# Optimization experiments

Hardware: AMD Instinct MI355X
Metric: run time of the kernel (lower is better)

## Reference

```python
import jax, jax.numpy as jnp
import numpy as np

N = 50000      # n_nodes
E = 800000     # n_edges
IN_NF = 64     # in_node_nf
HID = 128      # hidden_nf
OUT_NF = 64    # out_node_nf
L = 4          # n_layers
EH = HID // 2  # edge MLP hidden width (edge_nf_ratio=2)
C = 1.0        # aggregation scaling constant


def _w(k, shape):
    # fan-in scaled init (matches nn.Linear scale roughly)
    return jax.random.normal(k, shape, dtype=jnp.float32) / np.sqrt(shape[-2]).astype(np.float32)


def setup_inputs() -> dict:
    key = jax.random.key(0)
    ks = jax.random.split(key, 10)
    h = jax.random.normal(ks[0], (N, IN_NF), dtype=jnp.float32)
    edges = jax.random.randint(ks[1], (2, E), 0, N, dtype=jnp.int32)
    return {
        "h": h,
        "edges": edges,
        "W_in": _w(ks[2], (IN_NF, HID)),
        "b_in": jnp.zeros((HID,), jnp.float32),
        # stacked per-layer GCL params, leading dim L
        "eW1": _w(ks[3], (L, 2 * HID, EH)),
        "eb1": jnp.zeros((L, EH), jnp.float32),
        "eW2": _w(ks[4], (L, EH, EH)),
        "eb2": jnp.zeros((L, EH), jnp.float32),
        "nW1": _w(ks[5], (L, HID + EH, HID)),
        "nb1": jnp.zeros((L, HID), jnp.float32),
        "nW2": _w(ks[6], (L, HID, HID)),
        "nb2": jnp.zeros((L, HID), jnp.float32),
        "W_out": _w(ks[7], (HID, OUT_NF)),
        "b_out": jnp.zeros((OUT_NF,), jnp.float32),
    }


def reference(h, edges, W_in, b_in, eW1, eb1, eW2, eb2, nW1, nb1, nW2, nb2, W_out, b_out):
    row, col = edges[0], edges[1]
    h = h @ W_in + b_in  # [N, HID] embedding_in

    def layer(hc, p):
        w1, b1, w2, b2, m1, c1, m2, c2 = p
        # edge model: gather endpoints, concat, 2-layer SiLU MLP
        m = jnp.concatenate([hc[row], hc[col]], axis=1)          # [E, 2*HID]
        m = jax.nn.silu(m @ w1 + b1)                             # [E, EH]
        m = jax.nn.silu(m @ w2 + b2)                             # [E, EH]
        # node model: scatter-sum messages to source nodes, scale by C
        agg = jax.ops.segment_sum(m, row, num_segments=N) * C    # [N, EH]
        z = jnp.concatenate([hc, agg], axis=1)                   # [N, HID+EH]
        z = jax.nn.silu(z @ m1 + c1)
        z = z @ m2 + c2                                          # [N, HID]
        return hc + z, None  # residual=True

    h, _ = jax.lax.scan(layer, h, (eW1, eb1, eW2, eb2, nW1, nb1, nW2, nb2))
    return h @ W_out + b_out  # [N, OUT_NF] embedding_out
```

## Files before the change

kernel.cpp:

```cpp
#include <hip/hip_runtime.h>
#include <hip/hip_bf16.h>
#include <cstdint>
#include <cstddef>

#define N_NODES 50000
#define N_EDGES 800000
#define NR      50048
#define NBKT    196
#define BSH     8
#define BCHUNK  2048
#define CAP     6144

typedef __attribute__((ext_vector_type(8))) short short8;
typedef __attribute__((ext_vector_type(4))) float floatx4;
typedef __attribute__((ext_vector_type(4))) unsigned int uintx4;

__device__ inline float bf2f(unsigned short u) {
    union { unsigned int i; float f; } v; v.i = ((unsigned int)u) << 16; return v.f;
}
__device__ inline unsigned short f2bf(float f) {
    union { float f; unsigned int i; } v; v.f = f;
    unsigned int u = v.i;
    return (unsigned short)((u + 0x7FFFu + ((u >> 16) & 1u)) >> 16);
}
__device__ inline unsigned int f2bf_pk(float a, float b) {
    __hip_bfloat162 h2 = __float22bfloat162_rn(make_float2(a, b));
    return *reinterpret_cast<unsigned int*>(&h2);
}
__device__ inline float2 bf2f2(unsigned int u) {
    union { unsigned int i; float f; } lo, hi;
    lo.i = u << 16;
    hi.i = u & 0xFFFF0000u;
    return make_float2(lo.f, hi.f);
}
__device__ inline float silu_f(float x) {
    float e = __expf(-x);
    return x * __builtin_amdgcn_rcpf(1.0f + e);
}

__device__ inline int block_excl_scan_256(int v, int* buf) {
    int tid = threadIdx.x;
    buf[tid] = v;
    __syncthreads();
    #pragma unroll
    for (int off = 1; off < 256; off <<= 1) {
        int t = (tid >= off) ? buf[tid - off] : 0;
        __syncthreads();
        buf[tid] += t;
        __syncthreads();
    }
    return buf[tid] - v;
}

__device__ inline void pack_std(const float* __restrict__ src,
                                unsigned short* __restrict__ dst,
                                int NOUT, long j) {
    int i = (int)(j & 7);
    long rest = j >> 3;
    int n = (int)(rest % NOUT);
    int kb = (int)(rest / NOUT);
    dst[j] = f2bf(src[(long)(kb * 8 + i) * NOUT + n]);
}

#define NH0   (N_NODES * 64L)
#define SW_IN 8192L
#define SW_OUT 8192L
#define SW1   16384L
#define SE2   4096L
#define SN1   24576L
#define SN2   16384L
#define SB    128L
#define PERL  (SW1 + SE2 + SN1 + SN2 + SB)
#define PACK_TOTAL (NH0 + SW_IN + SW_OUT + 4 * PERL)

__global__ __launch_bounds__(256) void pack_kernel(
    const float* __restrict__ h0, const float* __restrict__ W_in,
    const float* __restrict__ W_out, const float* __restrict__ eW1,
    const float* __restrict__ eb1, const float* __restrict__ eW2,
    const float* __restrict__ nW1, const float* __restrict__ nW2,
    unsigned short* __restrict__ h0bf, unsigned short* __restrict__ Winp,
    unsigned short* __restrict__ Woutp, unsigned short* __restrict__ W1p,
    unsigned short* __restrict__ eW2p, unsigned short* __restrict__ nW1p,
    unsigned short* __restrict__ nW2p, float* __restrict__ biasP)
{
    long idx = (long)blockIdx.x * 256 + threadIdx.x;
    if (idx >= PACK_TOTAL) return;
    long j = idx;
    if (j < NH0) { h0bf[j] = f2bf(h0[j]); return; }
    j -= NH0;
    if (j < SW_IN) { pack_std(W_in, Winp, 128, j); return; }
    j -= SW_IN;
    if (j < SW_OUT) { pack_std(W_out, Woutp, 64, j); return; }
    j -= SW_OUT;
    int l = (int)(j / PERL);
    long r = j % PERL;
    if (r < SW1) {
        int i = (int)(r & 7);
        int n = (int)((r >> 3) & 127);
        int kb = (int)(r >> 10);
        int k = kb * 8 + i;
        const float* w = eW1 + (long)l * 256 * 64;
        float v = (n < 64) ? w[(long)k * 64 + n] : w[(long)(128 + k) * 64 + (n - 64)];
        W1p[(long)l * SW1 + r] = f2bf(v);
        return;
    }
    r -= SW1;
    if (r < SE2) { pack_std(eW2 + (long)l * 4096, eW2p + (long)l * SE2, 64, r); return; }
    r -= SE2;
    if (r < SN1) { pack_std(nW1 + (long)l * 24576, nW1p + (long)l * SN1, 128, r); return; }
    r -= SN1;
    if (r < SN2) { pack_std(nW2 + (long)l * 16384, nW2p + (long)l * SN2, 128, r); return; }
    r -= SN2;
    biasP[(long)l * 128 + r] = (r < 64) ? eb1[(long)l * 64 + r] : 0.0f;
}

__global__ __launch_bounds__(256) void hist_k(const int* __restrict__ erow,
                                              int* __restrict__ countB, int E) {
    __shared__ int c[NBKT];
    for (int i = threadIdx.x; i < NBKT; i += 256) c[i] = 0;
    __syncthreads();
    int j = blockIdx.x * BCHUNK + threadIdx.x;
    #pragma unroll
    for (int i = 0; i < BCHUNK / 256; i++, j += 256)
        if (j < E) atomicAdd(&c[erow[j] >> BSH], 1);
    __syncthreads();
    for (int i = threadIdx.x; i < NBKT; i += 256)
        if (c[i]) atomicAdd(&countB[i], c[i]);
}

__global__ __launch_bounds__(256) void bucket_scan_k(const int* __restrict__ countB,
                                                     int* __restrict__ bucketBase,
                                                     int* __restrict__ bucketCursor) {
    __shared__ int buf[256];
    int tid = threadIdx.x;
    int v = (tid < NBKT) ? countB[tid] : 0;
    int excl = block_excl_scan_256(v, buf);
    if (tid < NBKT) {
        bucketBase[tid] = excl;
        bucketCursor[tid] = excl;
    }
    if (tid == NBKT - 1) bucketBase[NBKT] = excl + v;
}

__global__ __launch_bounds__(256) void bin_k(
    const int* __restrict__ erow, const int* __restrict__ ecol,
    int* __restrict__ bucketCursor, int2* __restrict__ binned, int E)
{
    __shared__ int2 staged[BCHUNK];
    __shared__ int cnt[NBKT];
    __shared__ int binStart[NBKT];
    __shared__ int gbase[NBKT];
    __shared__ int scanbuf[256];
    const int tid = threadIdx.x;
    const int base = blockIdx.x * BCHUNK;
    const int nloc = min(BCHUNK, E - base);

    for (int i = tid; i < NBKT; i += 256) cnt[i] = 0;
    __syncthreads();

    int2 ed[BCHUNK / 256];
    int  bo[BCHUNK / 256];
    #pragma unroll
    for (int i = 0; i < BCHUNK / 256; i++) {
        int jl = i * 256 + tid;
        if (jl < nloc) {
            int j = base + jl;
            int r = erow[j], c = ecol[j];
            ed[i] = make_int2(r, c);
            int b = r >> BSH;
            int off = atomicAdd(&cnt[b], 1);
            bo[i] = (b << 12) | off;
        } else bo[i] = -1;
    }
    __syncthreads();

    int v = (tid < NBKT) ? cnt[tid] : 0;
    int excl = block_excl_scan_256(v, scanbuf);
    if (tid < NBKT) binStart[tid] = excl;
    if (tid < NBKT && v > 0) gbase[tid] = atomicAdd(&bucketCursor[tid], v);
    __syncthreads();

    #pragma unroll
    for (int i = 0; i < BCHUNK / 256; i++) {
        if (bo[i] >= 0)
            staged[binStart[bo[i] >> 12] + (bo[i] & 0xFFF)] = ed[i];
    }
    __syncthreads();

    for (int j = tid; j < nloc; j += 256) {
        int2 e = staged[j];
        int b = e.x >> BSH;
        binned[gbase[b] + (j - binStart[b])] = e;
    }
}

__global__ __launch_bounds__(256) void sort_k(
    const int2* __restrict__ binned, const int* __restrict__ bucketBase,
    int2* __restrict__ eidx)
{
    __shared__ int2 st[CAP];
    __shared__ int cnt[256];
    __shared__ int cur[256];
    __shared__ int scanbuf[256];
    const int b = blockIdx.x;
    const int tid = threadIdx.x;
    const int s0 = bucketBase[b];
    int n = bucketBase[b + 1] - s0;
    if (n > CAP) n = CAP;

    cnt[tid] = 0;
    __syncthreads();
    for (int j = tid; j < n; j += 256) {
        int2 e = binned[s0 + j];
        st[j] = e;
        atomicAdd(&cnt[e.x & 255], 1);
    }
    __syncthreads();
    int excl = block_excl_scan_256(cnt[tid], scanbuf);
    cur[tid] = excl;
    __syncthreads();
    for (int j = tid; j < n; j += 256) {
        int2 e = st[j];
        int pos = atomicAdd(&cur[e.x & 255], 1);
        eidx[s0 + pos] = e;
    }
}

__global__ __launch_bounds__(256) void edge_fused_k(
    const int2* __restrict__ eidx,
    const unsigned short* __restrict__ P,
    const unsigned short* __restrict__ Bp,
    const float* __restrict__ b2, float* __restrict__ agg, int E)
{
    __shared__ float M2s[64 * 68];
    __shared__ int ridS[64];
    __shared__ short segStartS[66];
    __shared__ int nsegS;
    const int tid = threadIdx.x;
    const int wave = tid >> 6;
    const int lane = tid & 63;
    const int lrow = lane & 15;
    const int quad = lane >> 4;
    const int e0 = blockIdx.x * 64;
    const int el = wave * 16 + lrow;
    const int e = e0 + el;

    short8 af0 = {0, 0, 0, 0, 0, 0, 0, 0};
    short8 af1 = af0;
    if (e < E) {
        int2 rc = eidx[e];
        int rr = rc.x, cc = rc.y;
        if (quad == 0) ridS[el] = rr;
        const uintx4* pt = (const uintx4*)(P + (size_t)rr * 128 + quad * 8);
        const uintx4* pb = (const uintx4*)(P + (size_t)cc * 128 + 64 + quad * 8);
        uintx4 t0 = pt[0], t1 = pt[4];
        uintx4 b0 = pb[0], b1 = pb[4];
        const unsigned int* t0u = (const unsigned int*)&t0;
        const unsigned int* t1u = (const unsigned int*)&t1;
        const unsigned int* b0u = (const unsigned int*)&b0;
        const unsigned int* b1u = (const unsigned int*)&b1;
        unsigned int o0[4], o1[4];
        #pragma unroll
        for (int i = 0; i < 4; i++) {
            float2 a0 = bf2f2(t0u[i]), c0 = bf2f2(b0u[i]);
            o0[i] = f2bf_pk(silu_f(a0.x + c0.x), silu_f(a0.y + c0.y));
            float2 a1 = bf2f2(t1u[i]), c1 = bf2f2(b1u[i]);
            o1[i] = f2bf_pk(silu_f(a1.x + c1.x), silu_f(a1.y + c1.y));
        }
        af0 = *(const short8*)o0;
        af1 = *(const short8*)o1;
    } else if (quad == 0) {
        ridS[el] = -1;
    }

    floatx4 acc[4];
    #pragma unroll
    for (int i = 0; i < 4; i++) acc[i] = (floatx4){0, 0, 0, 0};
    #pragma unroll
    for (int nt = 0; nt < 4; nt++) {
        short8 bf0 = *(const short8*)(Bp + (size_t)((0 * 4 + quad) * 64 + nt * 16 + lrow) * 8);
        acc[nt] = __builtin_amdgcn_mfma_f32_16x16x32_bf16(af0, bf0, acc[nt], 0, 0, 0);
        short8 bf1 = *(const short8*)(Bp + (size_t)((1 * 4 + quad) * 64 + nt * 16 + lrow) * 8);
        acc[nt] = __builtin_amdgcn_mfma_f32_16x16x32_bf16(af1, bf1, acc[nt], 0, 0, 0);
    }

    #pragma unroll
    for (int nt = 0; nt < 4; nt++) {
        int n = nt * 16 + lrow;
        float bv = b2[n];
        #pragma unroll
        for (int r = 0; r < 4; r++) {
            int el2 = wave * 16 + quad * 4 + r;
            M2s[el2 * 68 + n] = silu_f(acc[nt][r] + bv);
        }
    }
    __syncthreads();

    if (tid < 64) {
        bool st = (ridS[tid] >= 0) && (tid == 0 || ridS[tid] != ridS[tid - 1]);
        unsigned long long m = __ballot(st);
        if (st) {
            int pos = __popcll(m & ((1ull << tid) - 1));
            segStartS[pos] = (short)tid;
        }
        if (tid == 0) {
            int ns = __popcll(m);
            nsegS = ns;
            int nvalid = E - e0;
            if (nvalid > 64) nvalid = 64;
            segStartS[ns] = (short)nvalid;
        }
    }
    __syncthreads();

    {
        int f = tid & 63;
        int g = tid >> 6;
        int ns = nsegS;
        for (int j = g; j < ns; j += 4) {
            int a = segStartS[j], b = segStartS[j + 1];
            float s = 0.0f;
            for (int el2 = a; el2 < b; el2++) s += M2s[el2 * 68 + f];
            int rv = ridS[a];
            if (j == 0 || j == ns - 1)
                atomicAdd(&agg[(size_t)rv * 64 + f], s);
            else
                agg[(size_t)rv * 64 + f] = s;
        }
    }
}

#define SROW 264
template<int FINAL>
__global__ __launch_bounds__(512) void node_fused_k(
    const unsigned short* __restrict__ hbf, const float* __restrict__ agg,
    const unsigned short* __restrict__ W1, const float* __restrict__ b1,
    const unsigned short* __restrict__ W2, const float* __restrict__ b2,
    const unsigned short* __restrict__ B3, const float* __restrict__ bias3,
    float* __restrict__ hFT, unsigned short* __restrict__ hB,
    unsigned short* __restrict__ Pout, float* __restrict__ outF,
    float* __restrict__ aggZ, int M)
{
    __shared__ unsigned short S[64 * SROW];
    const int tid = threadIdx.x;
    const int m0 = blockIdx.x * 64;
    const int wave = tid >> 6;
    const int lane = tid & 63;
    const int lrow = lane & 15;
    const int quad = lane >> 4;
    const int g = wave >> 1;
    const int h = wave & 1;
    const int row0 = m0 + g * 16 + quad * 4;
    const int elb = g * 16 + quad * 4;

    short8 afa0, afa1;
    {
        const float* ap = agg + (size_t)(m0 + g * 16 + lrow) * 64;
        floatx4 q0 = *(const floatx4*)(ap + quad * 8);
        floatx4 q1 = *(const floatx4*)(ap + quad * 8 + 4);
        floatx4 q2 = *(const floatx4*)(ap + 32 + quad * 8);
        floatx4 q3 = *(const floatx4*)(ap + 32 + quad * 8 + 4);
        unsigned int c0[4] = { f2bf_pk(q0[0], q0[1]), f2bf_pk(q0[2], q0[3]),
                               f2bf_pk(q1[0], q1[1]), f2bf_pk(q1[2], q1[3]) };
        unsigned int c1[4] = { f2bf_pk(q2[0], q2[1]), f2bf_pk(q2[2], q2[3]),
                               f2bf_pk(q3[0], q3[1]), f2bf_pk(q3[2], q3[3]) };
        afa0 = *(const short8*)c0;
        afa1 = *(const short8*)c1;
    }

    floatx4 res4[4];
    #pragma unroll
    for (int j = 0; j < 4; j++) {
        int n = (4 * h + j) * 16 + lrow;
        res4[j] = *(const floatx4*)(hFT + (size_t)n * NR + row0);
    }

    for (int t = tid; t < 64 * 16; t += 512) {
        int rr = t >> 4, c = t & 15;
        int row = m0 + rr;
        uintx4 val = {0, 0, 0, 0};
        if (row < M) val = *(const uintx4*)(hbf + (size_t)row * 128 + c * 8);
        *(uintx4*)(&S[rr * SROW + c * 8]) = val;
    }
    __syncthreads();

    if (!FINAL) {
        floatx4 z = {0, 0, 0, 0};
        for (int t = tid; t < 64 * 16; t += 512) {
            int rr = t >> 4, c = t & 15;
            int row = m0 + rr;
            if (row < M) *(floatx4*)(aggZ + (size_t)row * 64 + c * 4) = z;
        }
    }

    const unsigned short* arow = &S[(g * 16 + lrow) * SROW];

    floatx4 acc[4];
    #pragma unroll
    for (int i = 0; i < 4; i++) acc[i] = (floatx4){0, 0, 0, 0};
    #pragma unroll
    for (int kt = 0; kt < 4; kt++) {
        short8 afrag = *(const short8*)(arow + kt * 32 + quad * 8);
        int kb = kt * 4 + quad;
        #pragma unroll
        for (int j = 0; j < 4; j++) {
            int n = (4 * h + j) * 16 + lrow;
            short8 bfrag = *(const short8*)(W1 + (size_t)(kb * 128 + n) * 8);
            acc[j] = __builtin_amdgcn_mfma_f32_16x16x32_bf16(afrag, bfrag, acc[j], 0, 0, 0);
        }
    }
    #pragma unroll
    for (int j = 0; j < 4; j++) {
        int n = (4 * h + j) * 16 + lrow;
        short8 b4 = *(const short8*)(W1 + (size_t)((16 + quad) * 128 + n) * 8);
        acc[j] = __builtin_amdgcn_mfma_f32_16x16x32_bf16(afa0, b4, acc[j], 0, 0, 0);
        short8 b5 = *(const short8*)(W1 + (size_t)((20 + quad) * 128 + n) * 8);
        acc[j] = __builtin_amdgcn_mfma_f32_16x16x32_bf16(afa1, b5, acc[j], 0, 0, 0);
    }

    #pragma unroll
    for (int j = 0; j < 4; j++) {
        int n = (4 * h + j) * 16 + lrow;
        float bv = b1[n];
        unsigned int p01 = f2bf_pk(silu_f(acc[j][0] + bv), silu_f(acc[j][1] + bv));
        unsigned int p23 = f2bf_pk(silu_f(acc[j][2] + bv), silu_f(acc[j][3] + bv));
        S[(elb + 0) * SROW + 128 + n] = (unsigned short)(p01 & 0xFFFF);
        S[(elb + 1) * SROW + 128 + n] = (unsigned short)(p01 >> 16);
        S[(elb + 2) * SROW + 128 + n] = (unsigned short)(p23 & 0xFFFF);
        S[(elb + 3) * SROW + 128 + n] = (unsigned short)(p23 >> 16);
    }
    __syncthreads();

    floatx4 acc2[4];
    #pragma unroll
    for (int i = 0; i < 4; i++) acc2[i] = (floatx4){0, 0, 0, 0};
    #pragma unroll
    for (int kt = 0; kt < 4; kt++) {
        short8 afrag = *(const short8*)(arow + 128 + kt * 32 + quad * 8);
        int kb = kt * 4 + quad;
        #pragma unroll
        for (int j = 0; j < 4; j++) {
            int n = (4 * h + j) * 16 + lrow;
            short8 bfrag = *(const short8*)(W2 + (size_t)(kb * 128 + n) * 8);
            acc2[j] = __builtin_amdgcn_mfma_f32_16x16x32_bf16(afrag, bfrag, acc2[j], 0, 0, 0);
        }
    }

    #pragma unroll
    for (int j = 0; j < 4; j++) {
        int n = (4 * h + j) * 16 + lrow;
        float bv = b2[n];
        floatx4 v4;
        #pragma unroll
        for (int r = 0; r < 4; r++) v4[r] = acc2[j][r] + bv + res4[j][r];
        unsigned int p01 = f2bf_pk(v4[0], v4[1]);
        unsigned int p23 = f2bf_pk(v4[2], v4[3]);
        S[(elb + 0) * SROW + n] = (unsigned short)(p01 & 0xFFFF);
        S[(elb + 1) * SROW + n] = (unsigned short)(p01 >> 16);
        S[(elb + 2) * SROW + n] = (unsigned short)(p23 & 0xFFFF);
        S[(elb + 3) * SROW + n] = (unsigned short)(p23 >> 16);
        if (!FINAL && row0 < M)
            *(floatx4*)(hFT + (size_t)n * NR + row0) = v4;
    }
    __syncthreads();

    constexpr int NT3 = FINAL ? 2 : 4;
    constexpr int NO3 = FINAL ? 64 : 128;
    floatx4 acc3[NT3];
    #pragma unroll
    for (int i = 0; i < NT3; i++) acc3[i] = (floatx4){0, 0, 0, 0};
    #pragma unroll
    for (int kt = 0; kt < 4; kt++) {
        short8 afrag = *(const short8*)(arow + kt * 32 + quad * 8);
        int kb = kt * 4 + quad;
        #pragma unroll
        for (int j = 0; j < NT3; j++) {
            int n = (NT3 * h + j) * 16 + lrow;
            short8 bfrag = *(const short8*)(B3 + (size_t)(kb * NO3 + n) * 8);
            acc3[j] = __builtin_amdgcn_mfma_f32_16x16x32_bf16(afrag, bfrag, acc3[j], 0, 0, 0);
        }
    }
    #pragma unroll
    for (int j = 0; j < NT3; j++) {
        int n = (NT3 * h + j) * 16 + lrow;
        float bv = bias3[n];
        if (FINAL) {
            #pragma unroll
            for (int r = 0; r < 4; r++)
                ((float*)(&S[(elb + r) * SROW + 128]))[n] = acc3[j][r] + bv;
        } else {
            unsigned int p01 = f2bf_pk(acc3[j][0] + bv, acc3[j][1] + bv);
            unsigned int p23 = f2bf_pk(acc3[j][2] + bv, acc3[j][3] + bv);
            S[(elb + 0) * SROW + 128 + n] = (unsigned short)(p01 & 0xFFFF);
            S[(elb + 1) * SROW + 128 + n] = (unsigned short)(p01 >> 16);
            S[(elb + 2) * SROW + 128 + n] = (unsigned short)(p23 & 0xFFFF);
            S[(elb + 3) * SROW + 128 + n] = (unsigned short)(p23 >> 16);
        }
    }
    __syncthreads();

    if (FINAL) {
        for (int t = tid; t < 64 * 16; t += 512) {
            int rr = t >> 4, c = t & 15;
            int row = m0 + rr;
            if (row < M)
                *(floatx4*)(outF + (size_t)row * 64 + c * 4) =
                    *(const floatx4*)((const float*)(&S[rr * SROW + 128]) + c * 4);
        }
    } else {
        for (int t = tid; t < 64 * 32; t += 512) {
            int rr = t >> 5, c = t & 31;
            int row = m0 + rr;
            if (row < M) {
                if (c < 16)
                    *(uintx4*)(hB + (size_t)row * 128 + c * 8) =
                        *(const uintx4*)(&S[rr * SROW + c * 8]);
                else
                    *(uintx4*)(Pout + (size_t)row * 128 + (c - 16) * 8) =
                        *(const uintx4*)(&S[rr * SROW + 128 + (c - 16) * 8]);
            }
        }
    }
}

#define SROWE 264
__global__ __launch_bounds__(256) void embed_fused_k(
    const unsigned short* __restrict__ h0bf, const unsigned short* __restrict__ Win,
    const float* __restrict__ b_in, const unsigned short* __restrict__ W1,
    const float* __restrict__ biasP, float* __restrict__ hFT,
    unsigned short* __restrict__ hB, unsigned short* __restrict__ Pout, int M)
{
    __shared__ unsigned short S[64 * SROWE];
    const int tid = threadIdx.x;
    const int m0 = blockIdx.x * 64;
    const int wave = tid >> 6;
    const int lane = tid & 63;
    const int lrow = lane & 15;
    const int quad = lane >> 4;
    const int row0 = m0 + wave * 16 + quad * 4;
    const int elb = wave * 16 + quad * 4;

    for (int t = tid; t < 64 * 8; t += 256) {
        int rr = t >> 3, c = t & 7;
        int row = m0 + rr;
        uintx4 val = {0, 0, 0, 0};
        if (row < M) val = *(const uintx4*)(h0bf + (size_t)row * 64 + c * 8);
        *(uintx4*)(&S[rr * SROWE + c * 8]) = val;
    }
    __syncthreads();

    const unsigned short* arow = &S[(wave * 16 + lrow) * SROWE];

    floatx4 acc[8];
    #pragma unroll
    for (int i = 0; i < 8; i++) acc[i] = (floatx4){0, 0, 0, 0};
    #pragma unroll
    for (int kt = 0; kt < 2; kt++) {
        short8 afrag = *(const short8*)(arow + kt * 32 + quad * 8);
        int kb = kt * 4 + quad;
        #pragma unroll
        for (int nt = 0; nt < 8; nt++) {
            short8 bfrag = *(const short8*)(Win + (size_t)(kb * 128 + nt * 16 + lrow) * 8);
            acc[nt] = __builtin_amdgcn_mfma_f32_16x16x32_bf16(afrag, bfrag, acc[nt], 0, 0, 0);
        }
    }

    #pragma unroll
    for (int nt = 0; nt < 8; nt++) {
        int n = nt * 16 + lrow;
        float bv = b_in[n];
        floatx4 v4;
        #pragma unroll
        for (int r = 0; r < 4; r++) v4[r] = acc[nt][r] + bv;
        unsigned int p01 = f2bf_pk(v4[0], v4[1]);
        unsigned int p23 = f2bf_pk(v4[2], v4[3]);
        S[(elb + 0) * SROWE + n] = (unsigned short)(p01 & 0xFFFF);
        S[(elb + 1) * SROWE + n] = (unsigned short)(p01 >> 16);
        S[(elb + 2) * SROWE + n] = (unsigned short)(p23 & 0xFFFF);
        S[(elb + 3) * SROWE + n] = (unsigned short)(p23 >> 16);
        if (row0 < M)
            *(floatx4*)(hFT + (size_t)n * NR + row0) = v4;
    }

    floatx4 acc3[8];
    #pragma unroll
    for (int i = 0; i < 8; i++) acc3[i] = (floatx4){0, 0, 0, 0};
    #pragma unroll
    for (int kt = 0; kt < 4; kt++) {
        short8 afrag = *(const short8*)(arow + kt * 32 + quad * 8);
        int kb = kt * 4 + quad;
        #pragma unroll
        for (int nt = 0; nt < 8; nt++) {
            short8 bfrag = *(const short8*)(W1 + (size_t)(kb * 128 + nt * 16 + lrow) * 8);
            acc3[nt] = __builtin_amdgcn_mfma_f32_16x16x32_bf16(afrag, bfrag, acc3[nt], 0, 0, 0);
        }
    }
    #pragma unroll
    for (int nt = 0; nt < 8; nt++) {
        int n = nt * 16 + lrow;
        float bv = biasP[n];
        unsigned int p01 = f2bf_pk(acc3[nt][0] + bv, acc3[nt][1] + bv);
        unsigned int p23 = f2bf_pk(acc3[nt][2] + bv, acc3[nt][3] + bv);
        S[(elb + 0) * SROWE + 128 + n] = (unsigned short)(p01 & 0xFFFF);
        S[(elb + 1) * SROWE + 128 + n] = (unsigned short)(p01 >> 16);
        S[(elb + 2) * SROWE + 128 + n] = (unsigned short)(p23 & 0xFFFF);
        S[(elb + 3) * SROWE + 128 + n] = (unsigned short)(p23 >> 16);
    }
    __syncthreads();

    for (int t = tid; t < 64 * 32; t += 256) {
        int rr = t / 32, c = t % 32;
        int row = m0 + rr;
        if (row < M) {
            if (c < 16)
                *(uintx4*)(hB + (size_t)row * 128 + c * 8) =
                    *(const uintx4*)(&S[rr * SROWE + c * 8]);
            else
                *(uintx4*)(Pout + (size_t)row * 128 + (c - 16) * 8) =
                    *(const uintx4*)(&S[rr * SROWE + 128 + (c - 16) * 8]);
        }
    }
}

extern "C" void kernel_launch(void* const* d_in, const int* in_sizes, int n_in,
                              void* d_out, int out_size, void* d_ws, size_t ws_size,
                              hipStream_t stream) {
    const float* h0   = (const float*)d_in[0];
    const int*   edges= (const int*)d_in[1];
    const float* W_in = (const float*)d_in[2];
    const float* b_in = (const float*)d_in[3];
    const float* eW1  = (const float*)d_in[4];
    const float* eb1  = (const float*)d_in[5];
    const float* eW2  = (const float*)d_in[6];
    const float* eb2  = (const float*)d_in[7];
    const float* nW1  = (const float*)d_in[8];
    const float* nb1  = (const float*)d_in[9];
    const float* nW2  = (const float*)d_in[10];
    const float* nb2  = (const float*)d_in[11];
    const float* W_out= (const float*)d_in[12];
    const float* b_out= (const float*)d_in[13];
    float* out = (float*)d_out;

    const int E = in_sizes[1] / 2;
    const int* erow = edges;
    const int* ecol = edges + E;

    char* ws = (char*)d_ws;
    unsigned short* hbf  = (unsigned short*)(ws + 0);
    float*          hFT  = (float*)(ws + 12800000);
    unsigned short* P    = (unsigned short*)(ws + 38424576);
    float*          agg  = (float*)(ws + 51224576);
    int2*           binned=(int2*)(ws + 51224576);
    unsigned short* h0bf = (unsigned short*)(ws + 76824576);
    int2*           eidx = (int2*)(ws + 76824576);
    float*          biasP= (float*)(ws + 83224576);
    unsigned short* Winp = (unsigned short*)(ws + 83226624);
    unsigned short* Woutp= (unsigned short*)(ws + 83243008);
    unsigned short* W1p  = (unsigned short*)(ws + 83259392);
    unsigned short* eW2p = (unsigned short*)(ws + 83390464);
    unsigned short* nW1p = (unsigned short*)(ws + 83423232);
    unsigned short* nW2p = (unsigned short*)(ws + 83619840);
    int*            countB=(int*)(ws + 83750912);
    int*            bucketBase=(int*)(ws + 83751936);
    int*            bucketCursor=(int*)(ws + 83752960);

    const int gemm_grid = (N_NODES + 63) / 64;
    const int edge_grid = (E + 63) / 64;
    const int pack_grid = (int)((PACK_TOTAL + 255) / 256);
    const int bin_grid  = (E + BCHUNK - 1) / BCHUNK;

    hipMemsetAsync(countB, 0, NBKT * 4, stream);
    pack_kernel<<<pack_grid, 256, 0, stream>>>(h0, W_in, W_out, eW1, eb1, eW2,
                                               nW1, nW2, h0bf, Winp, Woutp, W1p,
                                               eW2p, nW1p, nW2p, biasP);

    hist_k<<<bin_grid, 256, 0, stream>>>(erow, countB, E);
    bucket_scan_k<<<1, 256, 0, stream>>>(countB, bucketBase, bucketCursor);
    bin_k<<<bin_grid, 256, 0, stream>>>(erow, ecol, bucketCursor, binned, E);

    embed_fused_k<<<gemm_grid, 256, 0, stream>>>(
        h0bf, Winp, b_in, W1p, biasP, hFT, hbf, P, N_NODES);

    sort_k<<<NBKT, 256, 0, stream>>>(binned, bucketBase, eidx);

    hipMemsetAsync(agg, 0, (size_t)N_NODES * 64 * 4, stream);

    for (int l = 0; l < 4; l++) {
        edge_fused_k<<<edge_grid, 256, 0, stream>>>(
            eidx, P, eW2p + (size_t)l * SE2, eb2 + (size_t)l * 64, agg, E);
        if (l < 3) {
            node_fused_k<0><<<gemm_grid, 512, 0, stream>>>(
                hbf, agg, nW1p + (size_t)l * SN1, nb1 + (size_t)l * 128,
                nW2p + (size_t)l * SN2, nb2 + (size_t)l * 128,
                W1p + (size_t)(l + 1) * SW1, biasP + (size_t)(l + 1) * 128,
                hFT, hbf, P, nullptr, agg, N_NODES);
        } else {
            node_fused_k<1><<<gemm_grid, 512, 0, stream>>>(
                hbf, agg, nW1p + (size_t)l * SN1, nb1 + (size_t)l * 128,
                nW2p + (size_t)l * SN2, nb2 + (size_t)l * 128,
                Woutp, b_out, hFT, hbf, nullptr, out, nullptr, N_NODES);
        }
    }
}
```

Before: 434.8 us.

## Switch edge projections to fp16 with packed half SiLU and wave-local segment reduction

The per-node edge projections P and the second edge-layer weights are now stored in fp16 instead of bf16. The edge kernel computes the first SiLU with packed half2 math and runs the second GEMM through the f16 MFMA. The bias is folded into the accumulator init. The message tile is stored transposed, and the segment-start bookkeeping moves from shared memory into per-wave ballot bitmasks, which removes one block barrier and the serial segment scan. This cuts conversion ALU work and synchronisation in the hot edge kernel, at the cost of fp16 range and precision limits on activations, and pkrtz rounding.

After: 439.6 us. Within noise of the previous version (+1.1%).

```diff
diff --git a/kernel.cpp b/kernel.cpp
--- a/kernel.cpp
+++ b/kernel.cpp
@@ -1,5 +1,6 @@
 #include <hip/hip_runtime.h>
 #include <hip/hip_bf16.h>
+#include <hip/hip_fp16.h>
 #include <cstdint>
 #include <cstddef>
 
@@ -13,7 +14,9 @@
 
 typedef __attribute__((ext_vector_type(8))) short short8;
 typedef __attribute__((ext_vector_type(4))) float floatx4;
+typedef __attribute__((ext_vector_type(2))) float floatx2;
 typedef __attribute__((ext_vector_type(4))) unsigned int uintx4;
+typedef __attribute__((ext_vector_type(8))) _Float16 half8v;
 
 __device__ inline float bf2f(unsigned short u) {
     union { unsigned int i; float f; } v; v.i = ((unsigned int)u) << 16; return v.f;
@@ -32,6 +35,23 @@
     lo.i = u << 16;
     hi.i = u & 0xFFFF0000u;
     return make_float2(lo.f, hi.f);
+}
+__device__ inline unsigned short f2fh(float f) {
+    _Float16 h = (_Float16)f;
+    return __builtin_bit_cast(unsigned short, h);
+}
+__device__ inline unsigned int f2fh_pk(float a, float b) {
+    typedef __attribute__((ext_vector_type(2))) __fp16 h2v;
+    h2v r = __builtin_amdgcn_cvt_pkrtz(a, b);
+    return __builtin_bit_cast(unsigned int, r);
+}
+__device__ inline __half2 u2h(unsigned int u) { return __builtin_bit_cast(__half2, u); }
+__device__ inline unsigned int h2u(__half2 h) { return __builtin_bit_cast(unsigned int, h); }
+__device__ inline __half2 silu_h2(__half2 x) {
+    const __half2 nlog2e = __float2half2_rn(-1.4426950408889634f);
+    const __half2 one    = __float2half2_rn(1.0f);
+    __half2 e = h2exp2(__hmul2(x, nlog2e));
+    return __hmul2(x, h2rcp(__hadd2(e, one)));
 }
 __device__ inline float silu_f(float x) {
     float e = __expf(-x);
@@ -60,6 +80,15 @@
     int n = (int)(rest % NOUT);
     int kb = (int)(rest / NOUT);
     dst[j] = f2bf(src[(long)(kb * 8 + i) * NOUT + n]);
+}
+__device__ inline void pack_std_h(const float* __restrict__ src,
+                                  unsigned short* __restrict__ dst,
+                                  int NOUT, long j) {
+    int i = (int)(j & 7);
+    long rest = j >> 3;
+    int n = (int)(rest % NOUT);
+    int kb = (int)(rest / NOUT);
+    dst[j] = f2fh(src[(long)(kb * 8 + i) * NOUT + n]);
 }
 
 #define NH0   (N_NODES * 64L)
@@ -105,7 +134,7 @@
         return;
     }
     r -= SW1;
-    if (r < SE2) { pack_std(eW2 + (long)l * 4096, eW2p + (long)l * SE2, 64, r); return; }
+    if (r < SE2) { pack_std_h(eW2 + (long)l * 4096, eW2p + (long)l * SE2, 64, r); return; }
     r -= SE2;
     if (r < SN1) { pack_std(nW1 + (long)l * 24576, nW1p + (long)l * SN1, 128, r); return; }
     r -= SN1;
@@ -232,10 +261,8 @@
     const unsigned short* __restrict__ Bp,
     const float* __restrict__ b2, float* __restrict__ agg, int E)
 {
-    __shared__ float M2s[64 * 68];
+    __shared__ float M2s[64 * 66];
     __shared__ int ridS[64];
-    __shared__ short segStartS[66];
-    __shared__ int nsegS;
     const int tid = threadIdx.x;
     const int wave = tid >> 6;
     const int lane = tid & 63;
@@ -245,8 +272,15 @@
     const int el = wave * 16 + lrow;
     const int e = e0 + el;
 
-    short8 af0 = {0, 0, 0, 0, 0, 0, 0, 0};
-    short8 af1 = af0;
+    floatx4 acc[4];
+    #pragma unroll
+    for (int nt = 0; nt < 4; nt++) {
+        float bv = b2[nt * 16 + lrow];
+        acc[nt] = (floatx4){bv, bv, bv, bv};
+    }
+
+    half8v af0 = {};
+    half8v af1 = {};
     if (e < E) {
         int2 rc = eidx[e];
         int rr = rc.x, cc = rc.y;
@@ -255,77 +289,68 @@
         const uintx4* pb = (const uintx4*)(P + (size_t)cc * 128 + 64 + quad * 8);
         uintx4 t0 = pt[0], t1 = pt[4];
         uintx4 b0 = pb[0], b1 = pb[4];
-        const unsigned int* t0u = (const unsigned int*)&t0;
-        const unsigned int* t1u = (const unsigned int*)&t1;
-        const unsigned int* b0u = (const unsigned int*)&b0;
-        const unsigned int* b1u = (const unsigned int*)&b1;
-        unsigned int o0[4], o1[4];
+        uintx4 O0, O1;
         #pragma unroll
         for (int i = 0; i < 4; i++) {
-            float2 a0 = bf2f2(t0u[i]), c0 = bf2f2(b0u[i]);
-            o0[i] = f2bf_pk(silu_f(a0.x + c0.x), silu_f(a0.y + c0.y));
-            float2 a1 = bf2f2(t1u[i]), c1 = bf2f2(b1u[i]);
-            o1[i] = f2bf_pk(silu_f(a1.x + c1.x), silu_f(a1.y + c1.y));
-        }
-        af0 = *(const short8*)o0;
-        af1 = *(const short8*)o1;
+            O0[i] = h2u(silu_h2(__hadd2(u2h(t0[i]), u2h(b0[i]))));
+            O1[i] = h2u(silu_h2(__hadd2(u2h(t1[i]), u2h(b1[i]))));
+        }
+        af0 = __builtin_bit_cast(half8v, O0);
+        af1 = __builtin_bit_cast(half8v, O1);
     } else if (quad == 0) {
         ridS[el] = -1;
     }
 
-    floatx4 acc[4];
-    #pragma unroll
-    for (int i = 0; i < 4; i++) acc[i] = (floatx4){0, 0, 0, 0};
     #pragma unroll
     for (int nt = 0; nt < 4; nt++) {
-        short8 bf0 = *(const short8*)(Bp + (size_t)((0 * 4 + quad) * 64 + nt * 16 + lrow) * 8);
-        acc[nt] = __builtin_amdgcn_mfma_f32_16x16x32_bf16(af0, bf0, acc[nt], 0, 0, 0);
-        short8 bf1 = *(const short8*)(Bp + (size_t)((1 * 4 + quad) * 64 + nt * 16 + lrow) * 8);
-        acc[nt] = __builtin_amdgcn_mfma_f32_16x16x32_bf16(af1, bf1, acc[nt], 0, 0, 0);
-    }
-
+        half8v bf0 = *(const half8v*)(Bp + (size_t)((0 * 4 + quad) * 64 + nt * 16 + lrow) * 8);
+        acc[nt] = __builtin_amdgcn_mfma_f32_16x16x32_f16(af0, bf0, acc[nt], 0, 0, 0);
+        half8v bf1 = *(const half8v*)(Bp + (size_t)((1 * 4 + quad) * 64 + nt * 16 + lrow) * 8);
+        acc[nt] = __builtin_amdgcn_mfma_f32_16x16x32_f16(af1, bf1, acc[nt], 0, 0, 0);
+    }
+
+    const int elb = wave * 16 + quad * 4;
     #pragma unroll
     for (int nt = 0; nt < 4; nt++) {
         int n = nt * 16 + lrow;
-        float bv = b2[n];
-        #pragma unroll
-        for (int r = 0; r < 4; r++) {
-            int el2 = wave * 16 + quad * 4 + r;
-            M2s[el2 * 68 + n] = silu_f(acc[nt][r] + bv);
-        }
-    }
-    __syncthreads();
-
-    if (tid < 64) {
-        bool st = (ridS[tid] >= 0) && (tid == 0 || ridS[tid] != ridS[tid - 1]);
+        float* dst = &M2s[n * 66 + elb];
+        floatx2 v01 = {silu_f(acc[nt][0]), silu_f(acc[nt][1])};
+        floatx2 v23 = {silu_f(acc[nt][2]), silu_f(acc[nt][3])};
+        *(floatx2*)(dst)     = v01;
+        *(floatx2*)(dst + 2) = v23;
+    }
+    __syncthreads();
+
+    {
+        int rid0 = ridS[lane];
+        bool st = (rid0 >= 0) && (lane == 0 || rid0 != ridS[lane - 1]);
         unsigned long long m = __ballot(st);
-        if (st) {
-            int pos = __popcll(m & ((1ull << tid) - 1));
-            segStartS[pos] = (short)tid;
-        }
-        if (tid == 0) {
-            int ns = __popcll(m);
-            nsegS = ns;
-            int nvalid = E - e0;
-            if (nvalid > 64) nvalid = 64;
-            segStartS[ns] = (short)nvalid;
-        }
-    }
-    __syncthreads();
-
-    {
-        int f = tid & 63;
-        int g = tid >> 6;
-        int ns = nsegS;
-        for (int j = g; j < ns; j += 4) {
-            int a = segStartS[j], b = segStartS[j + 1];
+        int ns = __popcll(m);
+        int nvalid = E - e0; if (nvalid > 64) nvalid = 64;
+        const float* Mf = &M2s[lane * 66];
+        unsigned long long mm = m;
+        for (int k = 0; k < wave && mm; k++) mm &= mm - 1;
+        int j = wave;
+        while (mm) {
+            int a = __builtin_ctzll(mm);
+            unsigned long long m2 = mm & (mm - 1);
+            int b = m2 ? __builtin_ctzll(m2) : nvalid;
             float s = 0.0f;
-            for (int el2 = a; el2 < b; el2++) s += M2s[el2 * 68 + f];
+            int el2 = a;
+            if (el2 & 1) { s += Mf[el2]; el2++; }
+            for (; el2 + 1 < b; el2 += 2) {
+                floatx2 v = *(const floatx2*)(Mf + el2);
+                s += v[0] + v[1];
+            }
+            if (el2 < b) s += Mf[el2];
             int rv = ridS[a];
             if (j == 0 || j == ns - 1)
-                atomicAdd(&agg[(size_t)rv * 64 + f], s);
+                atomicAdd(&agg[(size_t)rv * 64 + lane], s);
             else
-                agg[(size_t)rv * 64 + f] = s;
+                agg[(size_t)rv * 64 + lane] = s;
+            mm = m2;
+            for (int k = 0; k < 3 && mm; k++) mm &= mm - 1;
+            j += 4;
         }
     }
 }
@@ -489,8 +514,8 @@
             for (int r = 0; r < 4; r++)
                 ((float*)(&S[(elb + r) * SROW + 128]))[n] = acc3[j][r] + bv;
         } else {
-            unsigned int p01 = f2bf_pk(acc3[j][0] + bv, acc3[j][1] + bv);
-            unsigned int p23 = f2bf_pk(acc3[j][2] + bv, acc3[j][3] + bv);
+            unsigned int p01 = f2fh_pk(acc3[j][0] + bv, acc3[j][1] + bv);
+            unsigned int p23 = f2fh_pk(acc3[j][2] + bv, acc3[j][3] + bv);
             S[(elb + 0) * SROW + 128 + n] = (unsigned short)(p01 & 0xFFFF);
             S[(elb + 1) * SROW + 128 + n] = (unsigned short)(p01 >> 16);
             S[(elb + 2) * SROW + 128 + n] = (unsigned short)(p23 & 0xFFFF);
@@ -599,8 +624,8 @@
     for (int nt = 0; nt < 8; nt++) {
         int n = nt * 16 + lrow;
         float bv = biasP[n];
-        unsigned int p01 = f2bf_pk(acc3[nt][0] + bv, acc3[nt][1] + bv);
-        unsigned int p23 = f2bf_pk(acc3[nt][2] + bv, acc3[nt][3] + bv);
+        unsigned int p01 = f2fh_pk(acc3[nt][0] + bv, acc3[nt][1] + bv);
+        unsigned int p23 = f2fh_pk(acc3[nt][2] + bv, acc3[nt][3] + bv);
         S[(elb + 0) * SROWE + 128 + n] = (unsigned short)(p01 & 0xFFFF);
         S[(elb + 1) * SROWE + 128 + n] = (unsigned short)(p01 >> 16);
         S[(elb + 2) * SROWE + 128 + n] = (unsigned short)(p23 & 0xFFFF);
```
